# Optimization experiments

Hardware: AMD Instinct MI355X
Metric: run time of the kernel (lower is better)

The kernel has to match this reference:

```python
import jax, jax.numpy as jnp
import numpy as np

B, H, N, D = 4, 16, 2048, 64


def setup_inputs() -> dict:
    key = jax.random.key(0)
    kq, kk, kv, km, kb = jax.random.split(key, 5)
    q = jax.random.normal(kq, (B, H, N, D), dtype=jnp.float32)
    k = jax.random.normal(kk, (B, H, N, D), dtype=jnp.float32)
    v = jax.random.normal(kv, (B, H, N, D), dtype=jnp.float32)
    # mostly-True mask so no row is fully masked
    mask = jax.random.uniform(km, (B, 1, N, N)) > 0.1
    attn_bias = jax.random.normal(kb, (1, H, N, N), dtype=jnp.float32)
    return {"q": q, "k": k, "v": v, "mask": mask, "attn_bias": attn_bias}


def reference(q, k, v, mask, attn_bias):
    scale = q.shape[-1] ** -0.5
    # sim: [B,H,N,N]
    sim = jnp.einsum('bhid,bhjd->bhij', q, k) * scale
    sim = sim + attn_bias
    neg = -jnp.finfo(sim.dtype).max
    sim = jnp.where(mask, sim, neg)
    attn = jax.nn.softmax(sim, axis=-1)
    out = jnp.einsum('bhij,bhjd->bhid', attn, v)
    return out
```

## Files before the change

kernel.cpp:

```cpp
#include <hip/hip_runtime.h>
#include <hip/hip_bf16.h>

typedef __bf16 bf16_t;
typedef bf16_t bf16x8 __attribute__((ext_vector_type(8)));
typedef float  floatx4 __attribute__((ext_vector_type(4)));

constexpr int Bb = 4, Hh = 16, Nn = 2048, Dd = 64;
constexpr int BM = 64;
constexpr int BN = 64;
constexpr int WM = 16;
constexpr float SCALE = 0.125f;
constexpr float NEG   = -3.4028234663852886e38f;

__global__ __launch_bounds__(256, 4)
void attn_fwd(const float* __restrict__ qg,
              const float* __restrict__ kg,
              const float* __restrict__ vg,
              const void*  __restrict__ maskg,
              const float* __restrict__ biasg,
              float* __restrict__ outg)
{
    __shared__ bf16x8 k_lds[512];
    __shared__ bf16x8 v_lds[512];
    __shared__ bf16x8 p_lds[4][128];

    const int tid  = threadIdx.x;
    const int wave = tid >> 6;
    const int lane = tid & 63;
    const int ln   = lane & 15;
    const int lq   = lane >> 4;

    const int id = blockIdx.x;
    const int b  = id & 3;
    const int h  = (id >> 2) & 15;
    const int mt = id >> 6;

    const int probe = ((const int*)maskg)[lane];
    const bool mask_i32 = __all(probe == 0 || probe == 1);
    const int*           mi = (const int*)maskg;
    const unsigned char* mb = (const unsigned char*)maskg;

    const size_t head  = (size_t)(b*Hh + h) * Nn * Dd;
    const int    qbase = mt*BM + wave*WM;

    bf16x8 qa[2];
    {
        const float* qp = qg + head + (size_t)(qbase + ln)*Dd + lq*8;
        #pragma unroll
        for (int kk = 0; kk < 2; ++kk) {
            float4 f0 = *(const float4*)(qp + kk*32);
            float4 f1 = *(const float4*)(qp + kk*32 + 4);
            bf16x8 a;
            a[0]=(bf16_t)f0.x; a[1]=(bf16_t)f0.y; a[2]=(bf16_t)f0.z; a[3]=(bf16_t)f0.w;
            a[4]=(bf16_t)f1.x; a[5]=(bf16_t)f1.y; a[6]=(bf16_t)f1.z; a[7]=(bf16_t)f1.w;
            qa[kk] = a;
        }
    }

    floatx4 o_acc[4];
    #pragma unroll
    for (int i = 0; i < 4; ++i) o_acc[i] = (floatx4){0.f,0.f,0.f,0.f};
    float mx[4], lsum[4];
    #pragma unroll
    for (int r = 0; r < 4; ++r) { mx[r] = -__builtin_inff(); lsum[r] = 0.f; }

    const int skey = tid >> 2;
    const int sd0  = (tid & 3) * 16;
    const int sblk = skey >> 4, sn = skey & 15;
    const int vkk  = skey >> 5, vq = (skey >> 3) & 3, vj = skey & 7;
    bf16_t* vl = (bf16_t*)v_lds;
    bf16_t* pl = (bf16_t*)p_lds[wave];

    for (int kt = 0; kt < Nn/BN; ++kt) {
        __syncthreads();
        {
            const float* kp = kg + head + (size_t)(kt*BN + skey)*Dd + sd0;
            const float* vp = vg + head + (size_t)(kt*BN + skey)*Dd + sd0;
            float kvv[16], vvv[16];
            *(float4*)(kvv+ 0) = *(const float4*)(kp+ 0);
            *(float4*)(kvv+ 4) = *(const float4*)(kp+ 4);
            *(float4*)(kvv+ 8) = *(const float4*)(kp+ 8);
            *(float4*)(kvv+12) = *(const float4*)(kp+12);
            *(float4*)(vvv+ 0) = *(const float4*)(vp+ 0);
            *(float4*)(vvv+ 4) = *(const float4*)(vp+ 4);
            *(float4*)(vvv+ 8) = *(const float4*)(vp+ 8);
            *(float4*)(vvv+12) = *(const float4*)(vp+12);
            #pragma unroll
            for (int g = 0; g < 2; ++g) {
                const int dg = sd0 + g*8;
                const int kkg = dg >> 5, qg2 = (dg >> 3) & 3;
                bf16x8 c;
                #pragma unroll
                for (int j = 0; j < 8; ++j) c[j] = (bf16_t)kvv[g*8+j];
                k_lds[(sblk*2 + kkg)*64 + qg2*16 + sn] = c;
            }
            #pragma unroll
            for (int t = 0; t < 16; ++t) {
                const int d = sd0 + t;
                const int nb = d >> 4, nn2 = d & 15;
                vl[(((vkk*4 + nb)*64 + vq*16 + nn2) << 3) | vj] = (bf16_t)vvv[t];
            }
        }
        __syncthreads();

        floatx4 s_acc[4];
        #pragma unroll
        for (int i = 0; i < 4; ++i) s_acc[i] = (floatx4){0.f,0.f,0.f,0.f};
        #pragma unroll
        for (int blk = 0; blk < 4; ++blk)
            #pragma unroll
            for (int kk = 0; kk < 2; ++kk)
                s_acc[blk] = __builtin_amdgcn_mfma_f32_16x16x32_bf16(
                    qa[kk], k_lds[(blk*2+kk)*64 + lane], s_acc[blk], 0, 0, 0);

        float sv[4][4], rmax[4];
        const size_t col0 = (size_t)kt*BN + ln;
        #pragma unroll
        for (int r = 0; r < 4; ++r) {
            const int m = qbase + lq*4 + r;
            const size_t brow = ((size_t)h*Nn + m)*Nn + col0;
            const size_t mrow = ((size_t)b*Nn + m)*Nn + col0;
            rmax[r] = NEG;
            #pragma unroll
            for (int blk = 0; blk < 4; ++blk) {
                float val = s_acc[blk][r]*SCALE + biasg[brow + blk*16];
                const bool ok = mask_i32 ? (mi[mrow + blk*16] != 0)
                                         : (mb[mrow + blk*16] != 0);
                val = ok ? val : NEG;
                sv[r][blk] = val;
                rmax[r] = fmaxf(rmax[r], val);
            }
        }
        #pragma unroll
        for (int off = 1; off < 16; off <<= 1)
            #pragma unroll
            for (int r = 0; r < 4; ++r)
                rmax[r] = fmaxf(rmax[r], __shfl_xor(rmax[r], off, 64));

        float alph[4], rsum[4];
        bf16_t pb[4][4];
        #pragma unroll
        for (int r = 0; r < 4; ++r) {
            const float mnew = fmaxf(mx[r], rmax[r]);
            alph[r] = __expf(mx[r] - mnew);
            mx[r] = mnew;
            float s = 0.f;
            #pragma unroll
            for (int blk = 0; blk < 4; ++blk) {
                const bf16_t p = (bf16_t)__expf(sv[r][blk] - mnew);
                pb[r][blk] = p;
                s += (float)p;
            }
            rsum[r] = s;
        }
        #pragma unroll
        for (int off = 1; off < 16; off <<= 1)
            #pragma unroll
            for (int r = 0; r < 4; ++r)
                rsum[r] += __shfl_xor(rsum[r], off, 64);
        #pragma unroll
        for (int r = 0; r < 4; ++r) {
            lsum[r] = lsum[r]*alph[r] + rsum[r];
            #pragma unroll
            for (int nb = 0; nb < 4; ++nb)
                o_acc[nb][r] *= alph[r];
        }

        #pragma unroll
        for (int r = 0; r < 4; ++r) {
            const int m = lq*4 + r;
            #pragma unroll
            for (int blk = 0; blk < 4; ++blk) {
                const int key = blk*16 + ln;
                const int kk2 = key >> 5, q2 = (key >> 3) & 3, j2 = key & 7;
                pl[((kk2*64 + q2*16 + m) << 3) | j2] = pb[r][blk];
            }
        }
        __syncthreads();

        #pragma unroll
        for (int kk = 0; kk < 2; ++kk) {
            const bf16x8 pa = p_lds[wave][kk*64 + lane];
            #pragma unroll
            for (int nb = 0; nb < 4; ++nb)
                o_acc[nb] = __builtin_amdgcn_mfma_f32_16x16x32_bf16(
                    pa, v_lds[(kk*4+nb)*64 + lane], o_acc[nb], 0, 0, 0);
        }
    }

    #pragma unroll
    for (int r = 0; r < 4; ++r) {
        const int m = qbase + lq*4 + r;
        const float inv = 1.f / lsum[r];
        float* op = outg + head + (size_t)m*Dd + ln;
        #pragma unroll
        for (int nb = 0; nb < 4; ++nb)
            op[nb*16] = o_acc[nb][r] * inv;
    }
}

extern "C" void kernel_launch(void* const* d_in, const int* in_sizes, int n_in,
                              void* d_out, int out_size, void* d_ws, size_t ws_size,
                              hipStream_t stream) {
    const float* q    = (const float*)d_in[0];
    const float* k    = (const float*)d_in[1];
    const float* v    = (const float*)d_in[2];
    const void*  mask = d_in[3];
    const float* bias = (const float*)d_in[4];
    float* out = (float*)d_out;
    (void)in_sizes; (void)n_in; (void)out_size; (void)d_ws; (void)ws_size;

    const int grid = Bb * Hh * (Nn / BM);
    attn_fwd<<<grid, 256, 0, stream>>>(q, k, v, mask, bias, out);
}
```

Measured before the change: 1.029 ms.

## Double query tile to 128 rows with 8 waves and drop per-wave P barrier

Each block now covers 128 query rows using 512 threads (8 waves), so each K/V tile loaded into LDS serves twice as many queries. The K/V staging is remapped so every thread converts 8 elements instead of 16. The block-wide barrier before reading P from LDS is removed, because each wave only reads its own P slice. This roughly halves global/L2 traffic for K and V and cuts barrier overhead. The costs are larger blocks and fewer resident workgroups, and the kernel now depends on in-wave LDS ordering for correctness.

```diff
diff --git a/kernel.cpp b/kernel.cpp
--- a/kernel.cpp
+++ b/kernel.cpp
@@ -6,13 +6,13 @@
 typedef float  floatx4 __attribute__((ext_vector_type(4)));
 
 constexpr int Bb = 4, Hh = 16, Nn = 2048, Dd = 64;
-constexpr int BM = 64;
+constexpr int BM = 128;
 constexpr int BN = 64;
 constexpr int WM = 16;
 constexpr float SCALE = 0.125f;
 constexpr float NEG   = -3.4028234663852886e38f;
 
-__global__ __launch_bounds__(256, 4)
+__global__ __launch_bounds__(512, 4)
 void attn_fwd(const float* __restrict__ qg,
               const float* __restrict__ kg,
               const float* __restrict__ vg,
@@ -22,7 +22,7 @@
 {
     __shared__ bf16x8 k_lds[512];
     __shared__ bf16x8 v_lds[512];
-    __shared__ bf16x8 p_lds[4][128];
+    __shared__ bf16x8 p_lds[8][128];
 
     const int tid  = threadIdx.x;
     const int wave = tid >> 6;
@@ -64,10 +64,12 @@
     #pragma unroll
     for (int r = 0; r < 4; ++r) { mx[r] = -__builtin_inff(); lsum[r] = 0.f; }
 
-    const int skey = tid >> 2;
-    const int sd0  = (tid & 3) * 16;
+    const int skey = tid >> 3;
+    const int sd0  = (tid & 7) * 8;
     const int sblk = skey >> 4, sn = skey & 15;
+    const int kkg  = sd0 >> 5,  qg2 = (sd0 >> 3) & 3;
     const int vkk  = skey >> 5, vq = (skey >> 3) & 3, vj = skey & 7;
+    const int vnb  = sd0 >> 4;
     bf16_t* vl = (bf16_t*)v_lds;
     bf16_t* pl = (bf16_t*)p_lds[wave];
 
@@ -76,29 +78,21 @@
         {
             const float* kp = kg + head + (size_t)(kt*BN + skey)*Dd + sd0;
             const float* vp = vg + head + (size_t)(kt*BN + skey)*Dd + sd0;
-            float kvv[16], vvv[16];
-            *(float4*)(kvv+ 0) = *(const float4*)(kp+ 0);
-            *(float4*)(kvv+ 4) = *(const float4*)(kp+ 4);
-            *(float4*)(kvv+ 8) = *(const float4*)(kp+ 8);
-            *(float4*)(kvv+12) = *(const float4*)(kp+12);
-            *(float4*)(vvv+ 0) = *(const float4*)(vp+ 0);
-            *(float4*)(vvv+ 4) = *(const float4*)(vp+ 4);
-            *(float4*)(vvv+ 8) = *(const float4*)(vp+ 8);
-            *(float4*)(vvv+12) = *(const float4*)(vp+12);
-            #pragma unroll
-            for (int g = 0; g < 2; ++g) {
-                const int dg = sd0 + g*8;
-                const int kkg = dg >> 5, qg2 = (dg >> 3) & 3;
-                bf16x8 c;
-                #pragma unroll
-                for (int j = 0; j < 8; ++j) c[j] = (bf16_t)kvv[g*8+j];
-                k_lds[(sblk*2 + kkg)*64 + qg2*16 + sn] = c;
-            }
-            #pragma unroll
-            for (int t = 0; t < 16; ++t) {
-                const int d = sd0 + t;
-                const int nb = d >> 4, nn2 = d & 15;
-                vl[(((vkk*4 + nb)*64 + vq*16 + nn2) << 3) | vj] = (bf16_t)vvv[t];
+            float4 k0 = *(const float4*)(kp);
+            float4 k1 = *(const float4*)(kp + 4);
+            float4 v0 = *(const float4*)(vp);
+            float4 v1 = *(const float4*)(vp + 4);
+            bf16x8 c;
+            c[0]=(bf16_t)k0.x; c[1]=(bf16_t)k0.y; c[2]=(bf16_t)k0.z; c[3]=(bf16_t)k0.w;
+            c[4]=(bf16_t)k1.x; c[5]=(bf16_t)k1.y; c[6]=(bf16_t)k1.z; c[7]=(bf16_t)k1.w;
+            k_lds[(sblk*2 + kkg)*64 + qg2*16 + sn] = c;
+            float vvv[8];
+            *(float4*)(vvv)   = v0;
+            *(float4*)(vvv+4) = v1;
+            #pragma unroll
+            for (int t = 0; t < 8; ++t) {
+                const int nn2 = (sd0 & 8) + t;
+                vl[(((vkk*4 + vnb)*64 + vq*16 + nn2) << 3) | vj] = (bf16_t)vvv[t];
             }
         }
         __syncthreads();
@@ -176,7 +170,6 @@
                 pl[((kk2*64 + q2*16 + m) << 3) | j2] = pb[r][blk];
             }
         }
-        __syncthreads();
 
         #pragma unroll
         for (int kk = 0; kk < 2; ++kk) {
@@ -211,5 +204,5 @@
     (void)in_sizes; (void)n_in; (void)out_size; (void)d_ws; (void)ws_size;
 
     const int grid = Bb * Hh * (Nn / BM);
-    attn_fwd<<<grid, 256, 0, stream>>>(q, k, v, mask, bias, out);
+    attn_fwd<<<grid, 512, 0, stream>>>(q, k, v, mask, bias, out);
 }
```

After: 1.015 ms. No clear change (-1.3%).

## Transpose S MFMA to vectorize bias/mask loads and enlarge tiles to 128x128

Applied to the files above, without the earlier changes.

Swaps the MFMA operands so each lane holds four consecutive key columns of one query row. This lets bias and mask be read with float4/int4 (or packed byte) loads instead of scalar gathers, and cuts the row max/sum reductions to two cross-lane shuffles. It also doubles the query and key tiles to 128 with 512 threads per block, and reuses the per-wave P buffer in two halves. The cost is more registers per thread and an extra shuffle to redistribute alpha and lsum for the output accumulators. The per-wave P buffer is also rewritten within an iteration without a barrier.

```diff
diff --git a/kernel.cpp b/kernel.cpp
--- a/kernel.cpp
+++ b/kernel.cpp
@@ -6,13 +6,14 @@
 typedef float  floatx4 __attribute__((ext_vector_type(4)));
 
 constexpr int Bb = 4, Hh = 16, Nn = 2048, Dd = 64;
-constexpr int BM = 64;
-constexpr int BN = 64;
+constexpr int BM = 128;
+constexpr int BN = 128;
 constexpr int WM = 16;
+constexpr int NT = Nn / BN;
 constexpr float SCALE = 0.125f;
 constexpr float NEG   = -3.4028234663852886e38f;
 
-__global__ __launch_bounds__(256, 4)
+__global__ __launch_bounds__(512, 4)
 void attn_fwd(const float* __restrict__ qg,
               const float* __restrict__ kg,
               const float* __restrict__ vg,
@@ -20,9 +21,9 @@
               const float* __restrict__ biasg,
               float* __restrict__ outg)
 {
-    __shared__ bf16x8 k_lds[512];
-    __shared__ bf16x8 v_lds[512];
-    __shared__ bf16x8 p_lds[4][128];
+    __shared__ bf16x8 k_lds[1024];
+    __shared__ bf16x8 v_lds[1024];
+    __shared__ bf16x8 p_lds[8][128];
 
     const int tid  = threadIdx.x;
     const int wave = tid >> 6;
@@ -60,18 +61,21 @@
     floatx4 o_acc[4];
     #pragma unroll
     for (int i = 0; i < 4; ++i) o_acc[i] = (floatx4){0.f,0.f,0.f,0.f};
-    float mx[4], lsum[4];
-    #pragma unroll
-    for (int r = 0; r < 4; ++r) { mx[r] = -__builtin_inff(); lsum[r] = 0.f; }
+    float mx = -__builtin_inff();
+    float lsum = 0.f;
 
     const int skey = tid >> 2;
     const int sd0  = (tid & 3) * 16;
     const int sblk = skey >> 4, sn = skey & 15;
     const int vkk  = skey >> 5, vq = (skey >> 3) & 3, vj = skey & 7;
+    const int vnb  = sd0 >> 4;
     bf16_t* vl = (bf16_t*)v_lds;
     bf16_t* pl = (bf16_t*)p_lds[wave];
 
-    for (int kt = 0; kt < Nn/BN; ++kt) {
+    const size_t brow0 = ((size_t)h*Nn + (qbase + ln))*Nn + lq*4;
+    const size_t mrow0 = ((size_t)b*Nn + (qbase + ln))*Nn + lq*4;
+
+    for (int kt = 0; kt < NT; ++kt) {
         __syncthreads();
         {
             const float* kp = kg + head + (size_t)(kt*BN + skey)*Dd + sd0;
@@ -96,102 +100,102 @@
             }
             #pragma unroll
             for (int t = 0; t < 16; ++t) {
-                const int d = sd0 + t;
-                const int nb = d >> 4, nn2 = d & 15;
-                vl[(((vkk*4 + nb)*64 + vq*16 + nn2) << 3) | vj] = (bf16_t)vvv[t];
+                vl[(((vkk*4 + vnb)*64 + vq*16 + t) << 3) | vj] = (bf16_t)vvv[t];
             }
         }
         __syncthreads();
 
-        floatx4 s_acc[4];
-        #pragma unroll
-        for (int i = 0; i < 4; ++i) s_acc[i] = (floatx4){0.f,0.f,0.f,0.f};
-        #pragma unroll
-        for (int blk = 0; blk < 4; ++blk)
+        floatx4 s_acc[8];
+        #pragma unroll
+        for (int i = 0; i < 8; ++i) s_acc[i] = (floatx4){0.f,0.f,0.f,0.f};
+        #pragma unroll
+        for (int blk = 0; blk < 8; ++blk)
             #pragma unroll
             for (int kk = 0; kk < 2; ++kk)
                 s_acc[blk] = __builtin_amdgcn_mfma_f32_16x16x32_bf16(
-                    qa[kk], k_lds[(blk*2+kk)*64 + lane], s_acc[blk], 0, 0, 0);
-
-        float sv[4][4], rmax[4];
-        const size_t col0 = (size_t)kt*BN + ln;
+                    k_lds[(blk*2+kk)*64 + lane], qa[kk], s_acc[blk], 0, 0, 0);
+
+        {
+            const size_t brow = brow0 + (size_t)kt*BN;
+            const size_t mrow = mrow0 + (size_t)kt*BN;
+            #pragma unroll
+            for (int blk = 0; blk < 8; ++blk) {
+                float4 b4 = *(const float4*)(biasg + brow + blk*16);
+                float bfa[4] = {b4.x, b4.y, b4.z, b4.w};
+                int oka[4];
+                if (mask_i32) {
+                    int4 m4 = *(const int4*)(mi + mrow + blk*16);
+                    oka[0]=m4.x; oka[1]=m4.y; oka[2]=m4.z; oka[3]=m4.w;
+                } else {
+                    unsigned mu = *(const unsigned*)(mb + mrow + blk*16);
+                    oka[0]=mu&255; oka[1]=(mu>>8)&255; oka[2]=(mu>>16)&255; oka[3]=(mu>>24)&255;
+                }
+                #pragma unroll
+                for (int r = 0; r < 4; ++r) {
+                    s_acc[blk][r] = fmaf(s_acc[blk][r], SCALE, oka[r] ? bfa[r] : NEG);
+                }
+            }
+        }
+
+        float m0 = NEG;
+        #pragma unroll
+        for (int blk = 0; blk < 8; ++blk) {
+            const float a = fmaxf(fmaxf(s_acc[blk][0], s_acc[blk][1]),
+                                  fmaxf(s_acc[blk][2], s_acc[blk][3]));
+            m0 = fmaxf(m0, a);
+        }
+        m0 = fmaxf(m0, __shfl_xor(m0, 16, 64));
+        m0 = fmaxf(m0, __shfl_xor(m0, 32, 64));
+        const float mnew = fmaxf(mx, m0);
+        const float alph = __expf(mx - mnew);
+        mx = mnew;
+
+        float rsum = 0.f;
+        #pragma unroll
+        for (int blk = 0; blk < 8; ++blk)
+            #pragma unroll
+            for (int r = 0; r < 4; ++r) {
+                const float p = (float)(bf16_t)__expf(s_acc[blk][r] - mnew);
+                s_acc[blk][r] = p;
+                rsum += p;
+            }
+        rsum += __shfl_xor(rsum, 16, 64);
+        rsum += __shfl_xor(rsum, 32, 64);
+        lsum = lsum*alph + rsum;
+
         #pragma unroll
         for (int r = 0; r < 4; ++r) {
-            const int m = qbase + lq*4 + r;
-            const size_t brow = ((size_t)h*Nn + m)*Nn + col0;
-            const size_t mrow = ((size_t)b*Nn + m)*Nn + col0;
-            rmax[r] = NEG;
-            #pragma unroll
-            for (int blk = 0; blk < 4; ++blk) {
-                float val = s_acc[blk][r]*SCALE + biasg[brow + blk*16];
-                const bool ok = mask_i32 ? (mi[mrow + blk*16] != 0)
-                                         : (mb[mrow + blk*16] != 0);
-                val = ok ? val : NEG;
-                sv[r][blk] = val;
-                rmax[r] = fmaxf(rmax[r], val);
-            }
-        }
-        #pragma unroll
-        for (int off = 1; off < 16; off <<= 1)
-            #pragma unroll
-            for (int r = 0; r < 4; ++r)
-                rmax[r] = fmaxf(rmax[r], __shfl_xor(rmax[r], off, 64));
-
-        float alph[4], rsum[4];
-        bf16_t pb[4][4];
-        #pragma unroll
-        for (int r = 0; r < 4; ++r) {
-            const float mnew = fmaxf(mx[r], rmax[r]);
-            alph[r] = __expf(mx[r] - mnew);
-            mx[r] = mnew;
-            float s = 0.f;
-            #pragma unroll
-            for (int blk = 0; blk < 4; ++blk) {
-                const bf16_t p = (bf16_t)__expf(sv[r][blk] - mnew);
-                pb[r][blk] = p;
-                s += (float)p;
-            }
-            rsum[r] = s;
-        }
-        #pragma unroll
-        for (int off = 1; off < 16; off <<= 1)
-            #pragma unroll
-            for (int r = 0; r < 4; ++r)
-                rsum[r] += __shfl_xor(rsum[r], off, 64);
-        #pragma unroll
-        for (int r = 0; r < 4; ++r) {
-            lsum[r] = lsum[r]*alph[r] + rsum[r];
+            const float ar = __shfl(alph, lq*4 + r, 16);
             #pragma unroll
             for (int nb = 0; nb < 4; ++nb)
-                o_acc[nb][r] *= alph[r];
-        }
-
-        #pragma unroll
-        for (int r = 0; r < 4; ++r) {
-            const int m = lq*4 + r;
-            #pragma unroll
-            for (int blk = 0; blk < 4; ++blk) {
-                const int key = blk*16 + ln;
-                const int kk2 = key >> 5, q2 = (key >> 3) & 3, j2 = key & 7;
-                pl[((kk2*64 + q2*16 + m) << 3) | j2] = pb[r][blk];
-            }
-        }
-        __syncthreads();
-
-        #pragma unroll
-        for (int kk = 0; kk < 2; ++kk) {
-            const bf16x8 pa = p_lds[wave][kk*64 + lane];
-            #pragma unroll
-            for (int nb = 0; nb < 4; ++nb)
-                o_acc[nb] = __builtin_amdgcn_mfma_f32_16x16x32_bf16(
-                    pa, v_lds[(kk*4+nb)*64 + lane], o_acc[nb], 0, 0, 0);
+                o_acc[nb][r] *= ar;
+        }
+
+        #pragma unroll
+        for (int half = 0; half < 2; ++half) {
+            #pragma unroll
+            for (int blk = half*4; blk < half*4 + 4; ++blk)
+                #pragma unroll
+                for (int r = 0; r < 4; ++r) {
+                    const int key = blk*16 + lq*4 + r;
+                    pl[((((key>>5)&1)*64 + ((key>>3)&3)*16 + ln) << 3) | (key&7)]
+                        = (bf16_t)s_acc[blk][r];
+                }
+            #pragma unroll
+            for (int kk = half*2; kk < half*2 + 2; ++kk) {
+                const bf16x8 pa = p_lds[wave][(kk&1)*64 + lane];
+                #pragma unroll
+                for (int nb = 0; nb < 4; ++nb)
+                    o_acc[nb] = __builtin_amdgcn_mfma_f32_16x16x32_bf16(
+                        pa, v_lds[(kk*4+nb)*64 + lane], o_acc[nb], 0, 0, 0);
+            }
         }
     }
 
     #pragma unroll
     for (int r = 0; r < 4; ++r) {
         const int m = qbase + lq*4 + r;
-        const float inv = 1.f / lsum[r];
+        const float inv = 1.f / __shfl(lsum, lq*4 + r, 16);
         float* op = outg + head + (size_t)m*Dd + ln;
         #pragma unroll
         for (int nb = 0; nb < 4; ++nb)
@@ -211,5 +215,5 @@
     (void)in_sizes; (void)n_in; (void)out_size; (void)d_ws; (void)ws_size;
 
     const int grid = Bb * Hh * (Nn / BM);
-    attn_fwd<<<grid, 256, 0, stream>>>(q, k, v, mask, bias, out);
+    attn_fwd<<<grid, 512, 0, stream>>>(q, k, v, mask, bias, out);
 }
```

Result: faster. 901.9 us (-12.3%).
